# Kernel tuning notes

Measured on AMD Instinct MI355X. Metric: run time of the kernel, lower is better.

Reference implementation:

```python
import jax, jax.numpy as jnp
import numpy as np

NUM_LABELS = 64
START, END, PAD = 0, 1, 2
B, L, V, D = 128, 1024, 30000, 256


def make_transitions(key):
    # replicates CRF.init_weights
    t = jax.random.uniform(key, (NUM_LABELS, NUM_LABELS), minval=-0.1, maxval=0.1)
    t = t.at[:, START].set(-10000.0)
    t = t.at[END, :].set(-10000.0)
    t = t.at[PAD, :].set(-10000.0)
    t = t.at[:, PAD].set(-10000.0)
    t = t.at[PAD, PAD].set(0.0)
    t = t.at[PAD, END].set(0.0)
    return t.astype(jnp.float32)


def setup_inputs() -> dict:
    key = jax.random.key(0)
    k0, k1, k2, k3, k4 = jax.random.split(key, 5)
    x = jax.random.randint(k0, (B, L), 0, V)
    tags = jax.random.randint(k1, (B, L), 0, NUM_LABELS)
    mask = jnp.ones((B, L), dtype=jnp.float32)  # ignored by CRF (source passes mask=None)
    embed = jax.random.normal(k2, (V, D), dtype=jnp.float32)
    W = jax.random.normal(k3, (D, NUM_LABELS), dtype=jnp.float32) * 0.05
    b = jnp.zeros((NUM_LABELS,), dtype=jnp.float32)
    trans = make_transitions(k4)
    return {"x": x, "tags": tags, "mask": mask, "embed": embed, "W": W, "b": b, "trans": trans}


def _crf_nll(emissions, tags, trans):
    # emissions: [B, L, T]; tags: [B, L]; trans: [T, T]
    # NOTE: original CRF.forward ignores the user mask (passes mask=None ->
    # all-ones mask), so every position is valid and last tag is tags[:, -1].
    # gold path score
    e_scores = jnp.take_along_axis(emissions, tags[:, :, None], axis=2)[:, :, 0].sum(axis=1)
    t_scores = trans[tags[:, :-1], tags[:, 1:]].sum(axis=1)
    scores = e_scores + t_scores + trans[START, tags[:, 0]] + trans[tags[:, -1], END]
    # log partition: forward algorithm (log-space recursion over time)
    alpha0 = trans[START][None, :] + emissions[:, 0]  # [B, T]

    def step(alphas, emit_t):
        # alphas: [B, T_prev] -> logsumexp over previous tag
        new = jax.nn.logsumexp(alphas[:, :, None] + trans[None, :, :], axis=1) + emit_t
        return new, None

    alphas, _ = jax.lax.scan(step, alpha0, jnp.swapaxes(emissions[:, 1:], 0, 1))
    log_z = jax.nn.logsumexp(alphas + trans[:, END][None, :], axis=1)  # [B]
    return -jnp.sum(scores - log_z)


def reference(x, tags, mask, embed, W, b, trans):
    emissions = embed[x] @ W + b  # [B, L, T]
    return _crf_nll(emissions, tags, trans)
```

## Files before the change

### kernel.cpp

```cpp
#include <hip/hip_runtime.h>
#include <hip/hip_bf16.h>

#define B_ 128
#define L_ 1024
#define T_ 64

using short8 = __attribute__((ext_vector_type(8))) short;
using f32x4  = __attribute__((ext_vector_type(4))) float;
using f32x16 = __attribute__((ext_vector_type(16))) float;

static __device__ __forceinline__ unsigned short bfb(float x) {
  return __builtin_bit_cast(unsigned short, __float2bfloat16(x));
}
static __device__ __forceinline__ float asf(unsigned u) { return __builtin_bit_cast(float, u); }
static __device__ __forceinline__ float bf2f(unsigned short b) { return asf(((unsigned)b) << 16); }
static __device__ __forceinline__ unsigned pk2(float lo, float hi) {
  __hip_bfloat162 h = __float22bfloat162_rn(float2{lo, hi});
  unsigned u;
  __builtin_memcpy(&u, &h, 4);
  return u;
}
static __device__ __forceinline__ unsigned pk2t(float lo, float hi) {
  return __builtin_amdgcn_perm(__builtin_bit_cast(unsigned, hi),
                               __builtin_bit_cast(unsigned, lo), 0x07060302u);
}
static __device__ __forceinline__ void pswap(unsigned& x, unsigned& y) {
  asm("v_permlane32_swap_b32 %0, %1" : "+v"(x), "+v"(y));
}

__global__ __launch_bounds__(256) void k_prep(const float* __restrict__ trans,
                                              unsigned short* __restrict__ expET) {
  int t = blockIdx.x * 256 + threadIdx.x;
  expET[t] = bfb(__expf(trans[(t & 63) * T_ + (t >> 6)]));
}

__global__ __launch_bounds__(256) void k_emis(const int* __restrict__ x,
                                              const float* __restrict__ embed,
                                              const float* __restrict__ W,
                                              const float* __restrict__ bias,
                                              unsigned short* __restrict__ Fout) {
  __shared__ unsigned short Wsw[16384];
  for (int e = threadIdx.x; e < 16384; e += 256) {
    int k = e >> 6, n = e & 63;
    int idx = ((k >> 5) << 11) + ((n >> 4) << 9) + (((k >> 3) & 3) << 7) + ((n & 15) << 3) + (k & 7);
    Wsw[idx] = bfb(W[e]);
  }
  __syncthreads();
  const int L = threadIdx.x & 63, wv = threadIdx.x >> 6, m = L & 15, q = L >> 4;
  short8 Wf[8][4];
#pragma unroll
  for (int kk = 0; kk < 8; kk++)
#pragma unroll
    for (int u = 0; u < 4; u++)
      Wf[kk][u] = *(const short8*)&Wsw[kk * 2048 + u * 512 + q * 128 + m * 8];
  const float bj0 = bias[m], bj1 = bias[16 + m], bj2 = bias[32 + m], bj3 = bias[48 + m];
  for (int it = 0; it < 4; it++) {
    const int tokbase = ((blockIdx.x * 4 + wv) * 4 + it) * 16;
    const float* er = embed + (size_t)x[tokbase + m] * 256;
    f32x4 acc[4] = {{0.f,0.f,0.f,0.f},{0.f,0.f,0.f,0.f},{0.f,0.f,0.f,0.f},{0.f,0.f,0.f,0.f}};
#pragma unroll
    for (int kap = 0; kap < 8; kap++) {
      float4 p0 = *(const float4*)(er + 32 * kap + 8 * q);
      float4 p1 = *(const float4*)(er + 32 * kap + 8 * q + 4);
      unsigned u0 = pk2(p0.x, p0.y), u1 = pk2(p0.z, p0.w);
      unsigned u2 = pk2(p1.x, p1.y), u3 = pk2(p1.z, p1.w);
      short8 af = __builtin_bit_cast(short8, make_uint4(u0, u1, u2, u3));
#pragma unroll
      for (int u = 0; u < 4; u++)
        acc[u] = __builtin_amdgcn_mfma_f32_16x16x32_bf16(af, Wf[kap][u], acc[u], 0, 0, 0);
    }
#pragma unroll
    for (int r = 0; r < 4; r++) {
      float e0 = acc[0][r] + bj0, e1 = acc[1][r] + bj1;
      float e2 = acc[2][r] + bj2, e3 = acc[3][r] + bj3;
      float mr = fmaxf(fmaxf(e0, e1), fmaxf(e2, e3));
#pragma unroll
      for (int off = 1; off < 16; off <<= 1) mr = fmaxf(mr, __shfl_xor(mr, off));
      float x0 = __expf(e0 - mr), x1 = __expf(e1 - mr);
      float x2 = __expf(e2 - mr), x3 = __expf(e3 - mr);
      float sr = (x0 + x1) + (x2 + x3);
#pragma unroll
      for (int off = 1; off < 16; off <<= 1) sr += __shfl_xor(sr, off);
      float rs = 1.0f / sr;
      unsigned short* Fp = Fout + (size_t)(tokbase + 4 * q + r) * T_ + m;
      Fp[0]  = bfb(x0 * rs);
      Fp[16] = bfb(x1 * rs);
      Fp[32] = bfb(x2 * rs);
      Fp[48] = bfb(x3 * rs);
    }
  }
}

__global__ __launch_bounds__(64) void k_scan(const unsigned short* __restrict__ F,
                                             const unsigned short* __restrict__ expET,
                                             unsigned short* __restrict__ XT,
                                             float* __restrict__ rlog,
                                             int Cshift) {
  const int job = blockIdx.x;
  const int C = 1 << Cshift;
  const int c = job & (C - 1);
  const int b = job >> Cshift;
  const int K = (1023 + C - 1) >> Cshift;
  const int a = 1 + c * K;
  const int len = min(K, 1024 - a);
  const int L = threadIdx.x, nh = L & 31, hh = L >> 5;

  short8 Af[2][4];
#pragma unroll
  for (int I = 0; I < 2; I++)
#pragma unroll
    for (int kap = 0; kap < 4; kap++)
      Af[I][kap] = *(const short8*)(expET + (32 * I + nh) * T_ + 16 * kap + 8 * hh);

  unsigned Bf[4][2][4];
#pragma unroll
  for (int kap = 0; kap < 4; kap++)
#pragma unroll
    for (int J = 0; J < 2; J++)
#pragma unroll
      for (int dw = 0; dw < 4; dw++) {
        int k0 = 16 * kap + 8 * hh + 2 * dw, n = 32 * J + nh;
        unsigned u = 0;
        if (k0 == n) u = 0x3F80u;
        if (k0 + 1 == n) u = 0x3F800000u;
        Bf[kap][J][dw] = u;
      }

  const unsigned short* Fb = F + (size_t)b * (L_ * T_);
  uint2 Fc[2][4];
#pragma unroll
  for (int I = 0; I < 2; I++)
#pragma unroll
    for (int j = 0; j < 4; j++)
      Fc[I][j] = *(const uint2*)(Fb + (size_t)a * T_ + (16 * I + 4 * j + 2 * hh) * 2);

  float logacc = 0.f;
  const f32x16 Z = {};

  for (int s = 0; s < len; s++) {
    uint2 Fn[2][4];
    {
      const unsigned short* Frow = Fb + (size_t)(a + s + 1) * T_;
#pragma unroll
      for (int I = 0; I < 2; I++)
#pragma unroll
        for (int j = 0; j < 4; j++)
          Fn[I][j] = *(const uint2*)(Frow + (16 * I + 4 * j + 2 * hh) * 2);
    }
    const bool rn = ((s & 15) == 15);
    float rs = 1.0f;
#pragma unroll
    for (int J = 0; J < 2; J++) {
      f32x16 D[2];
#pragma unroll
      for (int I = 0; I < 2; I++) {
        short8 b0 = __builtin_bit_cast(short8,
            make_uint4(Bf[0][J][0], Bf[0][J][1], Bf[0][J][2], Bf[0][J][3]));
        f32x16 d = __builtin_amdgcn_mfma_f32_32x32x16_bf16(Af[I][0], b0, Z, 0, 0, 0);
#pragma unroll
        for (int kap = 1; kap < 4; kap++) {
          short8 bk = __builtin_bit_cast(short8,
              make_uint4(Bf[kap][J][0], Bf[kap][J][1], Bf[kap][J][2], Bf[kap][J][3]));
          d = __builtin_amdgcn_mfma_f32_32x32x16_bf16(Af[I][kap], bk, d, 0, 0, 0);
        }
        D[I] = d;
      }
#pragma unroll
      for (int I = 0; I < 2; I++)
#pragma unroll
        for (int j = 0; j < 4; j++) {
          uint2 g = Fc[I][j];
          float f0 = asf(g.x << 16), f1 = asf(g.x & 0xffff0000u);
          float f2 = asf(g.y << 16), f3 = asf(g.y & 0xffff0000u);
          D[I][4 * j + 0] *= f0;
          D[I][4 * j + 1] *= f1;
          D[I][4 * j + 2] *= f2;
          D[I][4 * j + 3] *= f3;
        }
      if (rn) {
        if (J == 0) {
          float mx = D[0][0];
#pragma unroll
          for (int I = 0; I < 2; I++)
#pragma unroll
            for (int r = 0; r < 16; r++) mx = fmaxf(mx, D[I][r]);
#pragma unroll
          for (int off = 1; off < 64; off <<= 1) mx = fmaxf(mx, __shfl_xor(mx, off));
          rs = 1.0f / mx;
          logacc += __logf(mx);
        }
#pragma unroll
        for (int I = 0; I < 2; I++)
#pragma unroll
          for (int r = 0; r < 16; r++) D[I][r] *= rs;
      }
      unsigned PDt[2][4][2];
#pragma unroll
      for (int I = 0; I < 2; I++)
#pragma unroll
        for (int j = 0; j < 4; j++) {
          PDt[I][j][0] = pk2t(D[I][4 * j + 0], D[I][4 * j + 1]);
          PDt[I][j][1] = pk2t(D[I][4 * j + 2], D[I][4 * j + 3]);
        }
      if (s == len - 1) {
        unsigned short* Xrow = XT + (size_t)job * 4096 + 32 * J + nh;
#pragma unroll
        for (int I = 0; I < 2; I++)
#pragma unroll
          for (int j = 0; j < 4; j++)
#pragma unroll
            for (int p = 0; p < 2; p++) {
              const int r = 32 * I + 8 * j + 4 * hh + 2 * p;
              Xrow[(size_t)r * 64] = (unsigned short)(PDt[I][j][p] & 0xffffu);
              Xrow[(size_t)(r + 1) * 64] = (unsigned short)(PDt[I][j][p] >> 16);
            }
      } else {
#pragma unroll
        for (int kap = 0; kap < 4; kap++) {
          const int Ip = kap >> 1, e2 = 2 * (kap & 1);
          unsigned x0 = PDt[Ip][e2][0], y0 = PDt[Ip][e2 + 1][0];
          unsigned x1 = PDt[Ip][e2][1], y1 = PDt[Ip][e2 + 1][1];
          pswap(x0, y0);
          pswap(x1, y1);
          Bf[kap][J][0] = x0;
          Bf[kap][J][1] = x1;
          Bf[kap][J][2] = y0;
          Bf[kap][J][3] = y1;
        }
      }
    }
#pragma unroll
    for (int I = 0; I < 2; I++)
#pragma unroll
      for (int j = 0; j < 4; j++) Fc[I][j] = Fn[I][j];
  }
  if (L == 0) rlog[job] = logacc;
}

__global__ __launch_bounds__(256) void k_apply(const unsigned short* __restrict__ XT,
                                               const float* __restrict__ rlog,
                                               const unsigned short* __restrict__ F,
                                               const float* __restrict__ trans,
                                               const int* __restrict__ tags,
                                               float* __restrict__ out, int Cshift) {
  const int b = blockIdx.x, tid = threadIdx.x;
  const int C = 1 << Cshift;
  __shared__ float sred[4];
  __shared__ __align__(16) float vS[64];
  const int* tg = tags + (size_t)b * L_;
  const unsigned short* Fu = F + (size_t)b * (L_ * T_);
  float acc = 0.f;
  for (int l = tid; l < L_; l += 256) {
    const int t = tg[l];
    acc += __logf(bf2f(Fu[(size_t)l * T_ + t]));
    if (l < L_ - 1) acc += trans[t * T_ + tg[l + 1]];
  }
#pragma unroll
  for (int off = 32; off > 0; off >>= 1) acc += __shfl_xor(acc, off);
  if ((tid & 63) == 0) sred[tid >> 6] = acc;
  __syncthreads();
  if (tid >= 64) return;
  const int i = tid;
  float score = (sred[0] + sred[1]) + (sred[2] + sred[3]);
  score += trans[tg[0]] + trans[tg[L_ - 1] * T_ + 1];
  float v = __expf(trans[i]) * bf2f(Fu[i]);
  float lacc = 0.f;
  vS[i] = v;
  const uint4* Xb = (const uint4*)XT + (size_t)b * C * 512;
  uint4 Xr[8];
#pragma unroll
  for (int t = 0; t < 8; t++) Xr[t] = Xb[i * 8 + t];
  for (int c = 0; c < C; c++) {
    uint4 Xn[8];
    if (c + 1 < C) {
#pragma unroll
      for (int t = 0; t < 8; t++) Xn[t] = Xb[(size_t)(c + 1) * 512 + i * 8 + t];
    }
    float nv = 0.f;
#pragma unroll
    for (int t = 0; t < 8; t++) {
      float4 va = *(const float4*)&vS[8 * t];
      float4 vb = *(const float4*)&vS[8 * t + 4];
      nv = fmaf(asf(Xr[t].x << 16), va.x, nv);
      nv = fmaf(asf(Xr[t].x & 0xffff0000u), va.y, nv);
      nv = fmaf(asf(Xr[t].y << 16), va.z, nv);
      nv = fmaf(asf(Xr[t].y & 0xffff0000u), va.w, nv);
      nv = fmaf(asf(Xr[t].z << 16), vb.x, nv);
      nv = fmaf(asf(Xr[t].z & 0xffff0000u), vb.y, nv);
      nv = fmaf(asf(Xr[t].w << 16), vb.z, nv);
      nv = fmaf(asf(Xr[t].w & 0xffff0000u), vb.w, nv);
    }
    float mx = nv;
#pragma unroll
    for (int off = 1; off < 64; off <<= 1) mx = fmaxf(mx, __shfl_xor(mx, off));
    v = nv * (1.0f / mx);
    lacc += __logf(mx) + rlog[b * C + c];
    vS[i] = v;
#pragma unroll
    for (int t = 0; t < 8; t++) Xr[t] = Xn[t];
  }
  float t2 = v * __expf(trans[i * T_ + 1]);
#pragma unroll
  for (int off = 1; off < 64; off <<= 1) t2 += __shfl_xor(t2, off);
  if (i == 0) {
    const float logz = lacc + __logf(t2);
    atomicAdd(out, -(score - logz));
  }
}

extern "C" void kernel_launch(void* const* d_in, const int* in_sizes, int n_in,
                              void* d_out, int out_size, void* d_ws, size_t ws_size,
                              hipStream_t stream) {
  const int* x = (const int*)d_in[0];
  const int* tags = (const int*)d_in[1];
  const float* embed = (const float*)d_in[3];
  const float* W = (const float*)d_in[4];
  const float* bias = (const float*)d_in[5];
  const float* trans = (const float*)d_in[6];

  const size_t fbytes = (size_t)B_ * L_ * T_ * 2;
  int Cshift = 5;
  while (Cshift > 0) {
    size_t need = fbytes + (((size_t)1 << Cshift) * 1048576)
                  + (((size_t)128 << Cshift) * 4)
                  + 8192;
    if (need <= ws_size) break;
    Cshift--;
  }
  const int C = 1 << Cshift;

  char* ws = (char*)d_ws;
  unsigned short* F = (unsigned short*)ws;
  unsigned short* XT = (unsigned short*)(ws + fbytes);
  float* rlog = (float*)(ws + fbytes + (size_t)C * 1048576);
  unsigned short* expET = (unsigned short*)((char*)rlog + (size_t)128 * C * 4);
  float* out = (float*)d_out;

  hipMemsetAsync(out, 0, sizeof(float), stream);
  k_prep<<<16, 256, 0, stream>>>(trans, expET);
  k_emis<<<512, 256, 0, stream>>>(x, embed, W, bias, F);
  k_scan<<<128 * C, 64, 0, stream>>>(F, expET, XT, rlog, Cshift);
  k_apply<<<B_, 256, 0, stream>>>(XT, rlog, F, trans, tags, out, Cshift);
}
```

Baseline: 223.6 us.

## Fuse emission GEMM into chunked scan kernel, keep emissions in LDS

The emission projection and softmax are now computed inside the scan kernel for each chunk's 32 tokens, staged in shared memory, and read directly by the MFMA recursion. This removes the global round-trip of the bf16 emission tensor and two kernel launches (prep and emis). Gold emission log-probs are written per position, and the first token's emission is recomputed in the apply kernel. In exchange, exp(trans) is recomputed per wave, W fragments are reloaded from LDS inside the loop, the chunk count is fixed at 32 with no workspace-size fallback, and scan blocks become 256 threads with larger LDS use.

```diff
diff --git a/kernel.cpp b/kernel.cpp
--- a/kernel.cpp
+++ b/kernel.cpp
@@ -4,6 +4,8 @@
 #define B_ 128
 #define L_ 1024
 #define T_ 64
+#define CSH 5
+#define C_ 32
 
 using short8 = __attribute__((ext_vector_type(8))) short;
 using f32x4  = __attribute__((ext_vector_type(4))) float;
@@ -28,35 +30,40 @@
   asm("v_permlane32_swap_b32 %0, %1" : "+v"(x), "+v"(y));
 }
 
-__global__ __launch_bounds__(256) void k_prep(const float* __restrict__ trans,
-                                              unsigned short* __restrict__ expET) {
-  int t = blockIdx.x * 256 + threadIdx.x;
-  expET[t] = bfb(__expf(trans[(t & 63) * T_ + (t >> 6)]));
-}
-
-__global__ __launch_bounds__(256) void k_emis(const int* __restrict__ x,
+__global__ __launch_bounds__(256) void k_scan(const int* __restrict__ x,
+                                              const int* __restrict__ tags,
                                               const float* __restrict__ embed,
                                               const float* __restrict__ W,
                                               const float* __restrict__ bias,
-                                              unsigned short* __restrict__ Fout) {
+                                              const float* __restrict__ trans,
+                                              unsigned short* __restrict__ XT,
+                                              float* __restrict__ rlog,
+                                              float* __restrict__ goldF) {
   __shared__ unsigned short Wsw[16384];
+  __shared__ __align__(16) unsigned short Ftile[4][2048];
   for (int e = threadIdx.x; e < 16384; e += 256) {
     int k = e >> 6, n = e & 63;
     int idx = ((k >> 5) << 11) + ((n >> 4) << 9) + (((k >> 3) & 3) << 7) + ((n & 15) << 3) + (k & 7);
     Wsw[idx] = bfb(W[e]);
   }
   __syncthreads();
-  const int L = threadIdx.x & 63, wv = threadIdx.x >> 6, m = L & 15, q = L >> 4;
-  short8 Wf[8][4];
-#pragma unroll
-  for (int kk = 0; kk < 8; kk++)
-#pragma unroll
-    for (int u = 0; u < 4; u++)
-      Wf[kk][u] = *(const short8*)&Wsw[kk * 2048 + u * 512 + q * 128 + m * 8];
+
+  const int wv = threadIdx.x >> 6, L = threadIdx.x & 63;
+  const int job = blockIdx.x * 4 + wv;
+  const int c = job & (C_ - 1);
+  const int b = job >> CSH;
+  const int K = (1023 + C_ - 1) >> CSH;
+  const int a = 1 + c * K;
+  const int len = min(K, 1024 - a);
+  const int nh = L & 31, hh = L >> 5;
+  const int m = L & 15, q = L >> 4;
+  unsigned short* Ft = Ftile[wv];
+
   const float bj0 = bias[m], bj1 = bias[16 + m], bj2 = bias[32 + m], bj3 = bias[48 + m];
-  for (int it = 0; it < 4; it++) {
-    const int tokbase = ((blockIdx.x * 4 + wv) * 4 + it) * 16;
-    const float* er = embed + (size_t)x[tokbase + m] * 256;
+  for (int p = 0; p < 2; p++) {
+    int tok = a + 16 * p + m;
+    if (tok > 1023) tok = 1023;
+    const float* er = embed + (size_t)x[b * 1024 + tok] * 256;
     f32x4 acc[4] = {{0.f,0.f,0.f,0.f},{0.f,0.f,0.f,0.f},{0.f,0.f,0.f,0.f},{0.f,0.f,0.f,0.f}};
 #pragma unroll
     for (int kap = 0; kap < 8; kap++) {
@@ -66,8 +73,10 @@
       unsigned u2 = pk2(p1.x, p1.y), u3 = pk2(p1.z, p1.w);
       short8 af = __builtin_bit_cast(short8, make_uint4(u0, u1, u2, u3));
 #pragma unroll
-      for (int u = 0; u < 4; u++)
-        acc[u] = __builtin_amdgcn_mfma_f32_16x16x32_bf16(af, Wf[kap][u], acc[u], 0, 0, 0);
+      for (int u = 0; u < 4; u++) {
+        short8 bf8 = *(const short8*)&Wsw[kap * 2048 + u * 512 + q * 128 + m * 8];
+        acc[u] = __builtin_amdgcn_mfma_f32_16x16x32_bf16(af, bf8, acc[u], 0, 0, 0);
+      }
     }
 #pragma unroll
     for (int r = 0; r < 4; r++) {
@@ -82,35 +91,31 @@
 #pragma unroll
       for (int off = 1; off < 16; off <<= 1) sr += __shfl_xor(sr, off);
       float rs = 1.0f / sr;
-      unsigned short* Fp = Fout + (size_t)(tokbase + 4 * q + r) * T_ + m;
-      Fp[0]  = bfb(x0 * rs);
-      Fp[16] = bfb(x1 * rs);
-      Fp[32] = bfb(x2 * rs);
-      Fp[48] = bfb(x3 * rs);
-    }
-  }
-}
-
-__global__ __launch_bounds__(64) void k_scan(const unsigned short* __restrict__ F,
-                                             const unsigned short* __restrict__ expET,
-                                             unsigned short* __restrict__ XT,
-                                             float* __restrict__ rlog,
-                                             int Cshift) {
-  const int job = blockIdx.x;
-  const int C = 1 << Cshift;
-  const int c = job & (C - 1);
-  const int b = job >> Cshift;
-  const int K = (1023 + C - 1) >> Cshift;
-  const int a = 1 + c * K;
-  const int len = min(K, 1024 - a);
-  const int L = threadIdx.x, nh = L & 31, hh = L >> 5;
+      const int row = 16 * p + 4 * q + r;
+      Ft[row * 64 + m]      = bfb(x0 * rs);
+      Ft[row * 64 + 16 + m] = bfb(x1 * rs);
+      Ft[row * 64 + 32 + m] = bfb(x2 * rs);
+      Ft[row * 64 + 48 + m] = bfb(x3 * rs);
+    }
+  }
+  if (L < len) {
+    const int tgv = tags[b * 1024 + a + L];
+    goldF[b * 1024 + a + L] = __logf(bf2f(Ft[L * 64 + tgv]));
+  }
 
   short8 Af[2][4];
 #pragma unroll
   for (int I = 0; I < 2; I++)
 #pragma unroll
-    for (int kap = 0; kap < 4; kap++)
-      Af[I][kap] = *(const short8*)(expET + (32 * I + nh) * T_ + 16 * kap + 8 * hh);
+    for (int kap = 0; kap < 4; kap++) {
+      short8 aa;
+#pragma unroll
+      for (int d = 0; d < 8; d++) {
+        const int k = 16 * kap + 8 * hh + d;
+        aa[d] = (short)bfb(__expf(trans[k * T_ + 32 * I + nh]));
+      }
+      Af[I][kap] = aa;
+    }
 
   unsigned Bf[4][2][4];
 #pragma unroll
@@ -126,27 +131,16 @@
         Bf[kap][J][dw] = u;
       }
 
-  const unsigned short* Fb = F + (size_t)b * (L_ * T_);
-  uint2 Fc[2][4];
-#pragma unroll
-  for (int I = 0; I < 2; I++)
-#pragma unroll
-    for (int j = 0; j < 4; j++)
-      Fc[I][j] = *(const uint2*)(Fb + (size_t)a * T_ + (16 * I + 4 * j + 2 * hh) * 2);
-
   float logacc = 0.f;
   const f32x16 Z = {};
 
   for (int s = 0; s < len; s++) {
-    uint2 Fn[2][4];
-    {
-      const unsigned short* Frow = Fb + (size_t)(a + s + 1) * T_;
-#pragma unroll
-      for (int I = 0; I < 2; I++)
-#pragma unroll
-        for (int j = 0; j < 4; j++)
-          Fn[I][j] = *(const uint2*)(Frow + (16 * I + 4 * j + 2 * hh) * 2);
-    }
+    uint2 Fc[2][4];
+#pragma unroll
+    for (int I = 0; I < 2; I++)
+#pragma unroll
+      for (int j = 0; j < 4; j++)
+        Fc[I][j] = *(const uint2*)&Ft[s * 64 + (16 * I + 4 * j + 2 * hh) * 2];
     const bool rn = ((s & 15) == 15);
     float rs = 1.0f;
 #pragma unroll
@@ -209,10 +203,10 @@
 #pragma unroll
           for (int j = 0; j < 4; j++)
 #pragma unroll
-            for (int p = 0; p < 2; p++) {
-              const int r = 32 * I + 8 * j + 4 * hh + 2 * p;
-              Xrow[(size_t)r * 64] = (unsigned short)(PDt[I][j][p] & 0xffffu);
-              Xrow[(size_t)(r + 1) * 64] = (unsigned short)(PDt[I][j][p] >> 16);
+            for (int pp = 0; pp < 2; pp++) {
+              const int r = 32 * I + 8 * j + 4 * hh + 2 * pp;
+              Xrow[(size_t)r * 64] = (unsigned short)(PDt[I][j][pp] & 0xffffu);
+              Xrow[(size_t)(r + 1) * 64] = (unsigned short)(PDt[I][j][pp] >> 16);
             }
       } else {
 #pragma unroll
@@ -229,31 +223,28 @@
         }
       }
     }
-#pragma unroll
-    for (int I = 0; I < 2; I++)
-#pragma unroll
-      for (int j = 0; j < 4; j++) Fc[I][j] = Fn[I][j];
   }
   if (L == 0) rlog[job] = logacc;
 }
 
 __global__ __launch_bounds__(256) void k_apply(const unsigned short* __restrict__ XT,
                                                const float* __restrict__ rlog,
-                                               const unsigned short* __restrict__ F,
+                                               const float* __restrict__ goldF,
+                                               const int* __restrict__ x,
+                                               const float* __restrict__ embed,
+                                               const float* __restrict__ W,
+                                               const float* __restrict__ bias,
                                                const float* __restrict__ trans,
                                                const int* __restrict__ tags,
-                                               float* __restrict__ out, int Cshift) {
+                                               float* __restrict__ out) {
   const int b = blockIdx.x, tid = threadIdx.x;
-  const int C = 1 << Cshift;
   __shared__ float sred[4];
   __shared__ __align__(16) float vS[64];
   const int* tg = tags + (size_t)b * L_;
-  const unsigned short* Fu = F + (size_t)b * (L_ * T_);
   float acc = 0.f;
   for (int l = tid; l < L_; l += 256) {
-    const int t = tg[l];
-    acc += __logf(bf2f(Fu[(size_t)l * T_ + t]));
-    if (l < L_ - 1) acc += trans[t * T_ + tg[l + 1]];
+    if (l > 0) acc += goldF[(size_t)b * L_ + l];
+    if (l < L_ - 1) acc += trans[tg[l] * T_ + tg[l + 1]];
   }
 #pragma unroll
   for (int off = 32; off > 0; off >>= 1) acc += __shfl_xor(acc, off);
@@ -262,17 +253,30 @@
   if (tid >= 64) return;
   const int i = tid;
   float score = (sred[0] + sred[1]) + (sred[2] + sred[3]);
-  score += trans[tg[0]] + trans[tg[L_ - 1] * T_ + 1];
-  float v = __expf(trans[i]) * bf2f(Fu[i]);
+  const float* er0 = embed + (size_t)x[(size_t)b * L_] * 256;
+  float e = bias[i];
+#pragma unroll 8
+  for (int d = 0; d < 256; d++) e = fmaf(er0[d], W[d * T_ + i], e);
+  float mr = e;
+#pragma unroll
+  for (int off = 1; off < 64; off <<= 1) mr = fmaxf(mr, __shfl_xor(mr, off));
+  float pex = __expf(e - mr);
+  float sr = pex;
+#pragma unroll
+  for (int off = 1; off < 64; off <<= 1) sr += __shfl_xor(sr, off);
+  const int t0 = tg[0];
+  score += (__shfl(e, t0) - mr) - __logf(sr);
+  score += trans[t0] + trans[tg[L_ - 1] * T_ + 1];
+  float v = __expf(trans[i]) * (pex / sr);
   float lacc = 0.f;
   vS[i] = v;
-  const uint4* Xb = (const uint4*)XT + (size_t)b * C * 512;
+  const uint4* Xb = (const uint4*)XT + (size_t)b * C_ * 512;
   uint4 Xr[8];
 #pragma unroll
   for (int t = 0; t < 8; t++) Xr[t] = Xb[i * 8 + t];
-  for (int c = 0; c < C; c++) {
+  for (int c = 0; c < C_; c++) {
     uint4 Xn[8];
-    if (c + 1 < C) {
+    if (c + 1 < C_) {
 #pragma unroll
       for (int t = 0; t < 8; t++) Xn[t] = Xb[(size_t)(c + 1) * 512 + i * 8 + t];
     }
@@ -294,7 +298,7 @@
 #pragma unroll
     for (int off = 1; off < 64; off <<= 1) mx = fmaxf(mx, __shfl_xor(mx, off));
     v = nv * (1.0f / mx);
-    lacc += __logf(mx) + rlog[b * C + c];
+    lacc += __logf(mx) + rlog[b * C_ + c];
     vS[i] = v;
 #pragma unroll
     for (int t = 0; t < 8; t++) Xr[t] = Xn[t];
@@ -318,27 +322,13 @@
   const float* bias = (const float*)d_in[5];
   const float* trans = (const float*)d_in[6];
 
-  const size_t fbytes = (size_t)B_ * L_ * T_ * 2;
-  int Cshift = 5;
-  while (Cshift > 0) {
-    size_t need = fbytes + (((size_t)1 << Cshift) * 1048576)
-                  + (((size_t)128 << Cshift) * 4)
-                  + 8192;
-    if (need <= ws_size) break;
-    Cshift--;
-  }
-  const int C = 1 << Cshift;
-
   char* ws = (char*)d_ws;
-  unsigned short* F = (unsigned short*)ws;
-  unsigned short* XT = (unsigned short*)(ws + fbytes);
-  float* rlog = (float*)(ws + fbytes + (size_t)C * 1048576);
-  unsigned short* expET = (unsigned short*)((char*)rlog + (size_t)128 * C * 4);
+  unsigned short* XT = (unsigned short*)ws;
+  float* rlog = (float*)(ws + (size_t)C_ * 1048576);
+  float* goldF = (float*)((char*)rlog + (size_t)128 * C_ * 4);
   float* out = (float*)d_out;
 
   hipMemsetAsync(out, 0, sizeof(float), stream);
-  k_prep<<<16, 256, 0, stream>>>(trans, expET);
-  k_emis<<<512, 256, 0, stream>>>(x, embed, W, bias, F);
-  k_scan<<<128 * C, 64, 0, stream>>>(F, expET, XT, rlog, Cshift);
-  k_apply<<<B_, 256, 0, stream>>>(XT, rlog, F, trans, tags, out, Cshift);
-}
+  k_scan<<<32 * C_, 256, 0, stream>>>(x, tags, embed, W, bias, trans, XT, rlog, goldF);
+  k_apply<<<B_, 256, 0, stream>>>(XT, rlog, goldF, x, embed, W, bias, trans, tags, out);
+}
```

After: 210.1 us. 1.06x faster.
